# Performance work log

Measured on AMD Instinct MI355X. Metric: run time of the kernel, lower is better.

Reference implementation:

```python
import jax, jax.numpy as jnp
import numpy as np

B = 8192          # batch size
D = 128           # embedding_dim
R = 1000          # relation_dict_len
MARGIN = 1.0


def setup_inputs() -> dict:
    key = jax.random.key(0)
    k1, k2, k3, k4 = jax.random.split(key, 4)
    return {
        "positive_batch": jax.random.normal(k1, (B, 3, D), dtype=jnp.float32),
        "negative_batch": jax.random.normal(k2, (B, 3, D), dtype=jnp.float32),
        "r_idx": jax.random.randint(k3, (B,), 0, R),
        "rel_emb": jax.random.normal(k4, (R, D * D), dtype=jnp.float32),
    }


def _score(batch, Wr):
    # batch: (B, 3, D) -> h, r, t each (B, D); Wr: (B, D, D)
    h, r, t = batch[:, 0], batch[:, 1], batch[:, 2]
    d = jnp.abs(h + r - t)                       # (B, D)
    # x^T Wr x quadratic form per example, fused in one einsum
    return jnp.einsum('bi,bij,bj->b', d, Wr, d)  # (B,)


def reference(positive_batch, negative_batch, r_idx, rel_emb):
    # Gather per-example relation matrix (Wr built from positive relation,
    # reused for the negative score, as in the original module).
    Wr = rel_emb[r_idx].reshape(-1, D, D)        # (B, D, D)
    pos = _score(positive_batch, Wr)
    neg = _score(negative_batch, Wr)
    return jnp.mean(jax.nn.relu(MARGIN + pos - neg))
```

## Files before the change

### kernel.cpp

```cpp
#include <hip/hip_runtime.h>

#define BATCH 8192
#define DIM 128
#define NREL 1000
#define MARGIN 1.0f

#define WS_PARTIAL 0
#define WS_START   8192
#define WS_ORDER   9216

__global__ __launch_bounds__(1024) void sort_kernel(const int* __restrict__ r_idx,
                                                    int* __restrict__ start_g,
                                                    int* __restrict__ order) {
  __shared__ int s_cnt[1024];
  __shared__ int s_cur[1024];
  __shared__ int s_wsum[16];
  const int tid = threadIdx.x, lane = tid & 63, wave = tid >> 6;
  s_cnt[tid] = 0;
  __syncthreads();
  int my[8];
#pragma unroll
  for (int k = 0; k < 8; ++k) {
    my[k] = r_idx[tid + k * 1024];
    atomicAdd(&s_cnt[my[k]], 1);
  }
  __syncthreads();
  const int c = s_cnt[tid];
  int v = c;
#pragma unroll
  for (int o = 1; o < 64; o <<= 1) {
    int u = __shfl_up(v, o, 64);
    if (lane >= o) v += u;
  }
  if (lane == 63) s_wsum[wave] = v;
  __syncthreads();
  int woff = 0;
  for (int w = 0; w < wave; ++w) woff += s_wsum[w];
  const int my_start = woff + v - c;
  start_g[tid] = my_start;
  s_cur[tid] = my_start;
  __syncthreads();
#pragma unroll
  for (int k = 0; k < 8; ++k) {
    int p = atomicAdd(&s_cur[my[k]], 1);
    order[p] = tid + k * 1024;
  }
}

__device__ inline float2 dvec(const float* __restrict__ b, int c0) {
  float2 h = *(const float2*)(b + c0);
  float2 r = *(const float2*)(b + DIM + c0);
  float2 t = *(const float2*)(b + 2 * DIM + c0);
  return make_float2(fabsf(h.x + r.x - t.x), fabsf(h.y + r.y - t.y));
}

__global__ __launch_bounds__(256) void score_kernel(
    const float* __restrict__ pos_b, const float* __restrict__ neg_b,
    const float* __restrict__ rel_emb, const int* __restrict__ start,
    const int* __restrict__ order, float* __restrict__ partial) {
  __shared__ float s_d[64 * 36];
  __shared__ float s_ps[4][8];
  const int tid = threadIdx.x, lane = tid & 63, wave = tid >> 6;
  const int r = (blockIdx.x & 7) * (NREL / 8) + (blockIdx.x >> 3);
  const int sA = start[r], sB = start[r + 1];
  if (sA == sB) return;

  const int c0 = lane * 2;
  const int lam = lane & 31, rsel = lane >> 5;
  const int colb = lam * 4;
  const float* W = rel_emb + (size_t)r * (DIM * DIM) +
                   (size_t)(wave * 32 + rsel) * DIM + colb;
  const float* dbase = s_d + (wave * 16) * 36 + rsel * 16;

  for (int base = sA; base < sB; base += 8) {
    const int rem = sB - base;
    const int mm = rem < 8 ? rem : 8;

    {
      const int iA = 2 * wave, iB = iA + 1;
      const bool vA = iA < mm, vB = iB < mm;
      const float2 z = make_float2(0.f, 0.f);
      const int eA = vA ? order[base + iA] : 0;
      const int eB = vB ? order[base + iB] : 0;
      float2 dpA = vA ? dvec(pos_b + (size_t)eA * 3 * DIM, c0) : z;
      float2 dnA = vA ? dvec(neg_b + (size_t)eA * 3 * DIM, c0) : z;
      float2 dpB = vB ? dvec(pos_b + (size_t)eB * 3 * DIM, c0) : z;
      float2 dnB = vB ? dvec(neg_b + (size_t)eB * 3 * DIM, c0) : z;
      float* u = s_d + lane * 36;
      const int s2 = 2 * wave;
      *(float2*)(u + s2)      = make_float2(dpA.x, dpB.x);
      *(float2*)(u + 8 + s2)  = make_float2(dnA.x, dnB.x);
      *(float2*)(u + 16 + s2) = make_float2(dpA.y, dpB.y);
      *(float2*)(u + 24 + s2) = make_float2(dnA.y, dnB.y);
    }
    __syncthreads();

    const float4 fz = make_float4(0.f, 0.f, 0.f, 0.f);
    float4 ap[8], an[8];
#pragma unroll
    for (int i = 0; i < 8; ++i) { ap[i] = fz; an[i] = fz; }

#define FMA4(ACC, D, WV)          \
  ACC.x = fmaf(D, WV.x, ACC.x);   \
  ACC.y = fmaf(D, WV.y, ACC.y);   \
  ACC.z = fmaf(D, WV.z, ACC.z);   \
  ACC.w = fmaf(D, WV.w, ACC.w);

#pragma unroll 8
    for (int it = 0; it < 16; ++it) {
      float4 wv = *(const float4*)(W + (size_t)(it * 2) * DIM);
      const float* dd = dbase + it * 36;
      float4 p0 = *(const float4*)(dd + 0);
      float4 p1 = *(const float4*)(dd + 4);
      float4 n0 = *(const float4*)(dd + 8);
      float4 n1 = *(const float4*)(dd + 12);
      FMA4(ap[0], p0.x, wv) FMA4(ap[1], p0.y, wv)
      FMA4(ap[2], p0.z, wv) FMA4(ap[3], p0.w, wv)
      FMA4(ap[4], p1.x, wv) FMA4(ap[5], p1.y, wv)
      FMA4(ap[6], p1.z, wv) FMA4(ap[7], p1.w, wv)
      FMA4(an[0], n0.x, wv) FMA4(an[1], n0.y, wv)
      FMA4(an[2], n0.z, wv) FMA4(an[3], n0.w, wv)
      FMA4(an[4], n1.x, wv) FMA4(an[5], n1.y, wv)
      FMA4(an[6], n1.z, wv) FMA4(an[7], n1.w, wv)
    }
#undef FMA4

    float s[8];
#pragma unroll
    for (int i = 0; i < 8; ++i) s[i] = 0.f;
#define EPI(K, COMP)                                              \
    {                                                             \
      const int cc = colb + K;                                    \
      const float* dd = s_d + (cc >> 1) * 36 + (cc & 1) * 16;     \
      float4 plo = *(const float4*)(dd + 0);                      \
      float4 phi = *(const float4*)(dd + 4);                      \
      float4 nlo = *(const float4*)(dd + 8);                      \
      float4 nhi = *(const float4*)(dd + 12);                     \
      s[0] += ap[0].COMP * plo.x - an[0].COMP * nlo.x;            \
      s[1] += ap[1].COMP * plo.y - an[1].COMP * nlo.y;            \
      s[2] += ap[2].COMP * plo.z - an[2].COMP * nlo.z;            \
      s[3] += ap[3].COMP * plo.w - an[3].COMP * nlo.w;            \
      s[4] += ap[4].COMP * phi.x - an[4].COMP * nhi.x;            \
      s[5] += ap[5].COMP * phi.y - an[5].COMP * nhi.y;            \
      s[6] += ap[6].COMP * phi.z - an[6].COMP * nhi.z;            \
      s[7] += ap[7].COMP * phi.w - an[7].COMP * nhi.w;            \
    }
    EPI(0, x) EPI(1, y) EPI(2, z) EPI(3, w)
#undef EPI

#pragma unroll
    for (int o = 32; o > 0; o >>= 1) {
#pragma unroll
      for (int i = 0; i < 8; ++i) s[i] += __shfl_xor(s[i], o, 64);
    }
    if (lane == 0) {
#pragma unroll
      for (int i = 0; i < 8; ++i) s_ps[wave][i] = s[i];
    }
    __syncthreads();
    if (tid < mm)
      partial[order[base + tid]] =
          s_ps[0][tid] + s_ps[1][tid] + s_ps[2][tid] + s_ps[3][tid];
  }
}

__global__ __launch_bounds__(256) void reduce_kernel(const float* __restrict__ partial,
                                                     float* __restrict__ out) {
  float acc = 0.f;
  for (int i = threadIdx.x; i < BATCH; i += 256) {
    float v = MARGIN + partial[i];
    acc += (v > 0.f) ? v : 0.f;
  }
#pragma unroll
  for (int o = 32; o > 0; o >>= 1) acc += __shfl_xor(acc, o, 64);
  __shared__ float s[4];
  const int lane = threadIdx.x & 63, wave = threadIdx.x >> 6;
  if (lane == 0) s[wave] = acc;
  __syncthreads();
  if (threadIdx.x == 0) out[0] = (s[0] + s[1] + s[2] + s[3]) * (1.0f / BATCH);
}

extern "C" void kernel_launch(void* const* d_in, const int* in_sizes, int n_in,
                              void* d_out, int out_size, void* d_ws, size_t ws_size,
                              hipStream_t stream) {
  const float* pos_b = (const float*)d_in[0];
  const float* neg_b = (const float*)d_in[1];
  const int* r_idx = (const int*)d_in[2];
  const float* rel_emb = (const float*)d_in[3];
  float* out = (float*)d_out;

  float* partial = (float*)d_ws + WS_PARTIAL;
  int* start = (int*)d_ws + WS_START;
  int* order = (int*)d_ws + WS_ORDER;

  sort_kernel<<<1, 1024, 0, stream>>>(r_idx, start, order);
  score_kernel<<<NREL, 256, 0, stream>>>(pos_b, neg_b, rel_emb, start, order,
                                         partial);
  reduce_kernel<<<1, 256, 0, stream>>>(partial, out);
}
```

Measured before the change: 51.97 us.

## Split each relation's matrix rows across four blocks with per-segment partial scores

The score kernel now launches four blocks per relation. Each block handles a 32-row slice of the 128x128 relation matrix, so its inner loop drops from 16 to 4 iterations. Each block writes its partial quadratic-form result into a 4-wide per-example slot, and the reduce kernel sums the four slots before applying the hinge. The aim is more parallelism and more loads in flight across the GPU, since one block per relation underfilled it. The cost is that every block recomputes the difference vectors for its examples, repeating those pos/neg loads four times, and the workspace grows.

```diff
diff --git a/kernel.cpp b/kernel.cpp
--- a/kernel.cpp
+++ b/kernel.cpp
@@ -4,10 +4,12 @@
 #define DIM 128
 #define NREL 1000
 #define MARGIN 1.0f
+#define NSPLIT 4
+#define GRID (NREL * NSPLIT)
 
 #define WS_PARTIAL 0
-#define WS_START   8192
-#define WS_ORDER   9216
+#define WS_START   32768
+#define WS_ORDER   33792
 
 __global__ __launch_bounds__(1024) void sort_kernel(const int* __restrict__ r_idx,
                                                     int* __restrict__ start_g,
@@ -54,14 +56,16 @@
   return make_float2(fabsf(h.x + r.x - t.x), fabsf(h.y + r.y - t.y));
 }
 
-__global__ __launch_bounds__(256) void score_kernel(
+__global__ __launch_bounds__(256, 4) void score_kernel(
     const float* __restrict__ pos_b, const float* __restrict__ neg_b,
     const float* __restrict__ rel_emb, const int* __restrict__ start,
-    const int* __restrict__ order, float* __restrict__ partial) {
+    const int* __restrict__ order, float* __restrict__ partial4) {
   __shared__ float s_d[64 * 36];
   __shared__ float s_ps[4][8];
   const int tid = threadIdx.x, lane = tid & 63, wave = tid >> 6;
-  const int r = (blockIdx.x & 7) * (NREL / 8) + (blockIdx.x >> 3);
+  const int p = blockIdx.x;
+  const int r = (p & 7) * (NREL / 8) + (p >> 5);
+  const int seg = (p >> 3) & 3;
   const int sA = start[r], sB = start[r + 1];
   if (sA == sB) return;
 
@@ -69,8 +73,8 @@
   const int lam = lane & 31, rsel = lane >> 5;
   const int colb = lam * 4;
   const float* W = rel_emb + (size_t)r * (DIM * DIM) +
-                   (size_t)(wave * 32 + rsel) * DIM + colb;
-  const float* dbase = s_d + (wave * 16) * 36 + rsel * 16;
+                   (size_t)(seg * 32 + wave * 8 + rsel) * DIM + colb;
+  const float* dbase = s_d + (seg * 16 + wave * 4) * 36 + rsel * 16;
 
   for (int base = sA; base < sB; base += 8) {
     const int rem = sB - base;
@@ -106,8 +110,8 @@
   ACC.z = fmaf(D, WV.z, ACC.z);   \
   ACC.w = fmaf(D, WV.w, ACC.w);
 
-#pragma unroll 8
-    for (int it = 0; it < 16; ++it) {
+#pragma unroll
+    for (int it = 0; it < 4; ++it) {
       float4 wv = *(const float4*)(W + (size_t)(it * 2) * DIM);
       const float* dd = dbase + it * 36;
       float4 p0 = *(const float4*)(dd + 0);
@@ -159,16 +163,17 @@
     }
     __syncthreads();
     if (tid < mm)
-      partial[order[base + tid]] =
+      partial4[order[base + tid] * 4 + seg] =
           s_ps[0][tid] + s_ps[1][tid] + s_ps[2][tid] + s_ps[3][tid];
   }
 }
 
-__global__ __launch_bounds__(256) void reduce_kernel(const float* __restrict__ partial,
+__global__ __launch_bounds__(256) void reduce_kernel(const float* __restrict__ partial4,
                                                      float* __restrict__ out) {
   float acc = 0.f;
   for (int i = threadIdx.x; i < BATCH; i += 256) {
-    float v = MARGIN + partial[i];
+    float4 q = *(const float4*)(partial4 + i * 4);
+    float v = MARGIN + q.x + q.y + q.z + q.w;
     acc += (v > 0.f) ? v : 0.f;
   }
 #pragma unroll
@@ -189,12 +194,12 @@
   const float* rel_emb = (const float*)d_in[3];
   float* out = (float*)d_out;
 
-  float* partial = (float*)d_ws + WS_PARTIAL;
+  float* partial4 = (float*)d_ws + WS_PARTIAL;
   int* start = (int*)d_ws + WS_START;
   int* order = (int*)d_ws + WS_ORDER;
 
   sort_kernel<<<1, 1024, 0, stream>>>(r_idx, start, order);
-  score_kernel<<<NREL, 256, 0, stream>>>(pos_b, neg_b, rel_emb, start, order,
-                                         partial);
-  reduce_kernel<<<1, 256, 0, stream>>>(partial, out);
-}
+  score_kernel<<<GRID, 256, 0, stream>>>(pos_b, neg_b, rel_emb, start, order,
+                                         partial4);
+  reduce_kernel<<<1, 256, 0, stream>>>(partial4, out);
+}
```

Measured after the change: 56.43 us. 8.6% more time.
